# Kernel optimization log

Hardware: AMD Instinct MI355X
Metric: run time of the kernel (lower is better)

## Reference

```python
import jax, jax.numpy as jnp
import numpy as np

B, N, C, F = 8, 2048, 256, 128

def setup_inputs() -> dict:
    key = jax.random.key(0)
    ks = jax.random.split(key, 5)
    s = 0.02
    return {
        "x": jax.random.normal(ks[0], (B, N, C), dtype=jnp.float32),
        "Wf": jax.random.normal(ks[1], (C, F), dtype=jnp.float32) * s,
        "bf": jnp.zeros((F,), jnp.float32),
        "Wg": jax.random.normal(ks[2], (C, F), dtype=jnp.float32) * s,
        "bg": jnp.zeros((F,), jnp.float32),
        "Wh": jax.random.normal(ks[3], (C, F), dtype=jnp.float32) * s,
        "bh": jnp.zeros((F,), jnp.float32),
        "Wv": jax.random.normal(ks[4], (F, F), dtype=jnp.float32) * s,
        "bv": jnp.zeros((F,), jnp.float32),
    }

def reference(x, Wf, bf, Wg, bg, Wh, bh, Wv, bv):
    # 1x1 Conv1D == pointwise dense projection
    fx = x @ Wf + bf            # [B, N, F]
    gx = x @ Wg + bg            # [B, N, F]
    hx = x @ Wh + bh            # [B, N, F]
    # alpha = softmax(fx @ gx^T) over last axis -> [B, N, N]
    alpha = jax.nn.softmax(jnp.einsum('bnf,bmf->bnm', fx, gx), axis=-1)
    # o = hx^T @ alpha -> [B, F, N]
    o = jnp.einsum('bnf,bnm->bfm', hx, alpha)
    # faithful to original: RESHAPE (not transpose) to [B, N, F]
    o = o.reshape(B, N, F)
    return o @ Wv + bv          # [B, N, F]
```

## Files before the change

kernel.cpp:

```cpp
#include <hip/hip_runtime.h>
#include <hip/hip_bf16.h>


constexpr int Bb = 8, Nn = 2048, Cc = 256, Ff = 128;
constexpr long BNF = (long)Bb * Nn * Ff;
constexpr long BN  = (long)Bb * Nn;

typedef __bf16 bf16x8 __attribute__((ext_vector_type(8)));
typedef float  f32x4  __attribute__((ext_vector_type(4)));

__device__ inline unsigned short f2bf(float x) {
    unsigned u = __float_as_uint(x);
    unsigned r = (u + 0x7fffu + ((u >> 16) & 1u)) >> 16;
    return (unsigned short)r;
}
__device__ inline float bf2f(unsigned short h) {
    return __uint_as_float(((unsigned)h) << 16);
}


__global__ __launch_bounds__(256) void k_prepw(
    const float* __restrict__ W0, const float* __restrict__ W1,
    const float* __restrict__ W2,
    ushort* __restrict__ wth, ushort* __restrict__ wtl)
{
    __shared__ float ls[64][132];
    const float* W = (blockIdx.y == 0) ? W0 : (blockIdx.y == 1) ? W1 : W2;
    const int k0 = blockIdx.x * 64;
    const int t = threadIdx.x;
    const float4* src = (const float4*)(W + (size_t)k0 * 128);
    #pragma unroll
    for (int i = 0; i < 8; ++i) {
        int idx = t + 256 * i;
        int r = idx >> 5, c4 = idx & 31;
        *(float4*)&ls[r][c4 * 4] = src[idx];
    }
    __syncthreads();
    const int f = t >> 1, half = t & 1;
    __align__(16) ushort hb[32], lb[32];
    #pragma unroll
    for (int j = 0; j < 32; ++j) {
        float v = ls[half * 32 + j][f];
        ushort h = f2bf(v);
        hb[j] = h;
        lb[j] = f2bf(v - bf2f(h));
    }
    size_t base = ((size_t)blockIdx.y * 128 + f) * 256 + k0 + half * 32;
    #pragma unroll
    for (int j = 0; j < 4; ++j) {
        *(uint4*)&wth[base + j * 8] = *(const uint4*)&hb[j * 8];
        *(uint4*)&wtl[base + j * 8] = *(const uint4*)&lb[j * 8];
    }
}

__global__ __launch_bounds__(256) void k_prepwv(
    const float* __restrict__ Wv,
    ushort* __restrict__ wvth, ushort* __restrict__ wvtl)
{
    __shared__ float ls[64][132];
    const int k0 = blockIdx.x * 64;
    const int t = threadIdx.x;
    const float4* src = (const float4*)(Wv + (size_t)k0 * 128);
    #pragma unroll
    for (int i = 0; i < 8; ++i) {
        int idx = t + 256 * i;
        int r = idx >> 5, c4 = idx & 31;
        *(float4*)&ls[r][c4 * 4] = src[idx];
    }
    __syncthreads();
    const int f = t >> 1, half = t & 1;
    __align__(16) ushort hb[32], lb[32];
    #pragma unroll
    for (int j = 0; j < 32; ++j) {
        float v = ls[half * 32 + j][f];
        ushort h = f2bf(v);
        hb[j] = h;
        lb[j] = f2bf(v - bf2f(h));
    }
    size_t base = (size_t)f * 128 + k0 + half * 32;
    #pragma unroll
    for (int j = 0; j < 4; ++j) {
        *(uint4*)&wvth[base + j * 8] = *(const uint4*)&hb[j * 8];
        *(uint4*)&wvtl[base + j * 8] = *(const uint4*)&lb[j * 8];
    }
}

__global__ __launch_bounds__(512) void k_projm2(
    const float* __restrict__ x,
    const ushort* __restrict__ wth, const ushort* __restrict__ wtl,
    const float* __restrict__ b0, const float* __restrict__ b1,
    const float* __restrict__ b2,
    ushort* __restrict__ fxh, ushort* __restrict__ fxl,
    ushort* __restrict__ gxh, ushort* __restrict__ gxl,
    float* __restrict__ hxt)
{
    __shared__ ushort xsh[64][264], xsl[64][264];
    __shared__ float pmf[64][132];
    ushort (*pm)[136] = (ushort(*)[136])pmf;

    const int t = threadIdx.x;
    const long row0 = (long)blockIdx.x * 64;
    const int wid = t >> 6, lane = t & 63;
    const int wy = wid & 1, wx = wid >> 1;
    const int col = lane & 15, quad = lane >> 4;

    {
        #pragma unroll
        for (int i = 0; i < 8; ++i) {
            int idx = t + 512 * i;
            int r = idx >> 6, c4 = idx & 63;
            float4 v = *(const float4*)&x[(row0 + r) * 256 + c4 * 4];
            ushort4 h, l;
            h.x = f2bf(v.x); l.x = f2bf(v.x - bf2f(h.x));
            h.y = f2bf(v.y); l.y = f2bf(v.y - bf2f(h.y));
            h.z = f2bf(v.z); l.z = f2bf(v.z - bf2f(h.z));
            h.w = f2bf(v.w); l.w = f2bf(v.w - bf2f(h.w));
            *(ushort4*)&xsh[r][c4 * 4] = h;
            *(ushort4*)&xsl[r][c4 * 4] = l;
        }
    }
    __syncthreads();

    for (int y = 0; y < 3; ++y) {
        const ushort* Wh = wth + (size_t)y * 128 * 256;
        const ushort* Wl = wtl + (size_t)y * 128 * 256;
        const float* bias = (y == 0) ? b0 : (y == 1) ? b1 : b2;

        f32x4 acc[2][2];
        #pragma unroll
        for (int i = 0; i < 2; ++i)
            #pragma unroll
            for (int j = 0; j < 2; ++j) acc[i][j] = (f32x4){0.f, 0.f, 0.f, 0.f};

        #pragma unroll
        for (int kk = 0; kk < 8; ++kk) {
            const int ko = kk * 32 + quad * 8;
            bf16x8 ah[2], al[2], bh[2], bl[2];
            #pragma unroll
            for (int tn = 0; tn < 2; ++tn) {
                int r = wy * 32 + tn * 16 + col;
                ah[tn] = *(const bf16x8*)&xsh[r][ko];
                al[tn] = *(const bf16x8*)&xsl[r][ko];
            }
            #pragma unroll
            for (int tf = 0; tf < 2; ++tf) {
                int f = wx * 32 + tf * 16 + col;
                bh[tf] = *(const bf16x8*)&Wh[(size_t)f * 256 + ko];
                bl[tf] = *(const bf16x8*)&Wl[(size_t)f * 256 + ko];
            }
            #pragma unroll
            for (int tn = 0; tn < 2; ++tn)
                #pragma unroll
                for (int tf = 0; tf < 2; ++tf) {
                    acc[tn][tf] = __builtin_amdgcn_mfma_f32_16x16x32_bf16(ah[tn], bh[tf], acc[tn][tf], 0, 0, 0);
                    acc[tn][tf] = __builtin_amdgcn_mfma_f32_16x16x32_bf16(ah[tn], bl[tf], acc[tn][tf], 0, 0, 0);
                    acc[tn][tf] = __builtin_amdgcn_mfma_f32_16x16x32_bf16(al[tn], bh[tf], acc[tn][tf], 0, 0, 0);
                }
        }

        float v[2][2][4];
        #pragma unroll
        for (int tf = 0; tf < 2; ++tf) {
            float bb = bias[wx * 32 + tf * 16 + col];
            #pragma unroll
            for (int tn = 0; tn < 2; ++tn)
                #pragma unroll
                for (int r = 0; r < 4; ++r) v[tn][tf][r] = acc[tn][tf][r] + bb;
        }

        if (y == 2) {
            float* ob = hxt + (row0 >> 11) * (size_t)128 * 2048;
            int n0 = (int)(row0 & 2047);
            #pragma unroll
            for (int tn = 0; tn < 2; ++tn) {
                int n = n0 + wy * 32 + tn * 16 + quad * 4;
                #pragma unroll
                for (int tf = 0; tf < 2; ++tf) {
                    int f = wx * 32 + tf * 16 + col;
                    f32x4 vv = {v[tn][tf][0], v[tn][tf][1], v[tn][tf][2], v[tn][tf][3]};
                    *(f32x4*)&ob[(size_t)f * 2048 + n] = vv;
                }
            }
        } else {
            ushort* oh = (y == 0) ? fxh : gxh;
            ushort* ol = (y == 0) ? fxl : gxl;
            __syncthreads();
            #pragma unroll
            for (int tn = 0; tn < 2; ++tn)
                #pragma unroll
                for (int tf = 0; tf < 2; ++tf)
                    #pragma unroll
                    for (int r = 0; r < 4; ++r)
                        pm[wy * 32 + tn * 16 + quad * 4 + r][wx * 32 + tf * 16 + col] = f2bf(v[tn][tf][r]);
            __syncthreads();
            #pragma unroll
            for (int i = 0; i < 2; ++i) {
                int idx = t + 512 * i;
                int r = idx >> 4, c = idx & 15;
                *(uint4*)&oh[(row0 + r) * 128 + c * 8] = *(const uint4*)&pm[r][c * 8];
            }
            __syncthreads();
            #pragma unroll
            for (int tn = 0; tn < 2; ++tn)
                #pragma unroll
                for (int tf = 0; tf < 2; ++tf)
                    #pragma unroll
                    for (int r = 0; r < 4; ++r) {
                        float hv = bf2f(f2bf(v[tn][tf][r]));
                        pm[wy * 32 + tn * 16 + quad * 4 + r][wx * 32 + tf * 16 + col] = f2bf(v[tn][tf][r] - hv);
                    }
            __syncthreads();
            #pragma unroll
            for (int i = 0; i < 2; ++i) {
                int idx = t + 512 * i;
                int r = idx >> 4, c = idx & 15;
                *(uint4*)&ol[(row0 + r) * 128 + c * 8] = *(const uint4*)&pm[r][c * 8];
            }
            __syncthreads();
        }
    }
}

__global__ __launch_bounds__(512, 4) void k_score3(
    const ushort* __restrict__ fxh, const ushort* __restrict__ fxl,
    const ushort* __restrict__ gxh, const ushort* __restrict__ gxl,
    ushort* __restrict__ Pt, float* __restrict__ linv)
{
    __shared__ ushort gsh[64][136], gsl[64][136];
    __shared__ __align__(16) ushort fsbuf[2 * 64 * 136];
    __shared__ float lsum[64];
    ushort* fsh = fsbuf;
    ushort* fsl = fsbuf + 64 * 136;
    ushort* pm  = fsbuf;

    const int t = threadIdx.x;
    const int n0g = blockIdx.x * 64;
    const int b = n0g >> 11;
    const int n0 = n0g & 2047;
    const int wid = t >> 6, lane = t & 63;
    const int wy = wid & 1, wx = wid >> 1;
    const int col = lane & 15, quad = lane >> 4;

    {
        const uint4* sh = (const uint4*)(fxh + (size_t)n0g * 128);
        const uint4* sl = (const uint4*)(fxl + (size_t)n0g * 128);
        #pragma unroll
        for (int i = 0; i < 2; ++i) {
            int idx = t + 512 * i;
            int r = idx >> 4, c = idx & 15;
            *(uint4*)&fsh[r * 136 + c * 8] = sh[idx];
            *(uint4*)&fsl[r * 136 + c * 8] = sl[idx];
        }
        if (t < 64) lsum[t] = 0.f;
    }
    __syncthreads();

    bf16x8 Ah[4][2], Al[4][2];
    #pragma unroll
    for (int kk = 0; kk < 4; ++kk) {
        const int ko = kk * 32 + quad * 8;
        #pragma unroll
        for (int tn = 0; tn < 2; ++tn) {
            int r = wy * 32 + tn * 16 + col;
            Ah[kk][tn] = *(const bf16x8*)&fsh[r * 136 + ko];
            Al[kk][tn] = *(const bf16x8*)&fsl[r * 136 + ko];
        }
    }

    float rs[2][4] = {};
    const ushort* gbh = gxh + (size_t)b * 2048 * 128;
    const ushort* gbl = gxl + (size_t)b * 2048 * 128;
    ushort* Pb = Pt + (size_t)b * 2048 * 2048;

    for (int mt = 0; mt < 32; ++mt) {
        __syncthreads();
        {
            const uint4* sh = (const uint4*)(gbh + (size_t)mt * 64 * 128);
            const uint4* sl = (const uint4*)(gbl + (size_t)mt * 64 * 128);
            #pragma unroll
            for (int i = 0; i < 2; ++i) {
                int idx = t + 512 * i;
                int r = idx >> 4, c = idx & 15;
                *(uint4*)&gsh[r][c * 8] = sh[idx];
                *(uint4*)&gsl[r][c * 8] = sl[idx];
            }
        }
        __syncthreads();

        f32x4 acc[2];
        acc[0] = (f32x4){0.f, 0.f, 0.f, 0.f};
        acc[1] = (f32x4){0.f, 0.f, 0.f, 0.f};

        #pragma unroll
        for (int kk = 0; kk < 4; ++kk) {
            const int ko = kk * 32 + quad * 8;
            int r = wx * 16 + col;
            bf16x8 bh = *(const bf16x8*)&gsh[r][ko];
            bf16x8 bl = *(const bf16x8*)&gsl[r][ko];
            #pragma unroll
            for (int tn = 0; tn < 2; ++tn) {
                acc[tn] = __builtin_amdgcn_mfma_f32_16x16x32_bf16(Ah[kk][tn], bh, acc[tn], 0, 0, 0);
                acc[tn] = __builtin_amdgcn_mfma_f32_16x16x32_bf16(Ah[kk][tn], bl, acc[tn], 0, 0, 0);
                acc[tn] = __builtin_amdgcn_mfma_f32_16x16x32_bf16(Al[kk][tn], bh, acc[tn], 0, 0, 0);
            }
        }

        #pragma unroll
        for (int tn = 0; tn < 2; ++tn) {
            float e0 = __expf(acc[tn][0]);
            float e1 = __expf(acc[tn][1]);
            float e2 = __expf(acc[tn][2]);
            float e3 = __expf(acc[tn][3]);
            rs[tn][0] += e0; rs[tn][1] += e1; rs[tn][2] += e2; rs[tn][3] += e3;
            ushort4 pk;
            pk.x = f2bf(e0); pk.y = f2bf(e1); pk.z = f2bf(e2); pk.w = f2bf(e3);
            int ml = wx * 16 + col;
            int nl = wy * 32 + tn * 16 + quad * 4;
            *(ushort4*)&pm[ml * 72 + nl] = pk;
        }
        __syncthreads();
        {
            int r = t >> 3, c = t & 7;
            *(uint4*)&Pb[(size_t)(mt * 64 + r) * 2048 + n0 + c * 8] = *(const uint4*)&pm[r * 72 + c * 8];
        }
    }

    #pragma unroll
    for (int off = 1; off < 16; off <<= 1)
        #pragma unroll
        for (int tn = 0; tn < 2; ++tn)
            #pragma unroll
            for (int r = 0; r < 4; ++r) rs[tn][r] += __shfl_xor(rs[tn][r], off);
    if (col == 0) {
        #pragma unroll
        for (int tn = 0; tn < 2; ++tn)
            #pragma unroll
            for (int r = 0; r < 4; ++r)
                atomicAdd(&lsum[wy * 32 + tn * 16 + quad * 4 + r], rs[tn][r]);
    }
    __syncthreads();
    if (t < 64) linv[n0g + t] = 1.0f / lsum[t];
}

__global__ __launch_bounds__(256) void k_scaleh2(
    const float* __restrict__ hxt, const float* __restrict__ linv,
    ushort* __restrict__ hth, ushort* __restrict__ htl)
{
    const int t = threadIdx.x;
    const int bf = blockIdx.x;
    const int b = bf >> 7;
    const size_t base = (size_t)bf * 2048;
    const float* L = linv + (size_t)b * 2048;
    const int n = t * 8;
    float4 v0 = *(const float4*)&hxt[base + n];
    float4 v1 = *(const float4*)&hxt[base + n + 4];
    float4 l0 = *(const float4*)&L[n];
    float4 l1 = *(const float4*)&L[n + 4];
    float w[8] = {v0.x * l0.x, v0.y * l0.y, v0.z * l0.z, v0.w * l0.w,
                  v1.x * l1.x, v1.y * l1.y, v1.z * l1.z, v1.w * l1.w};
    __align__(16) ushort hb[8], lb[8];
    #pragma unroll
    for (int j = 0; j < 8; ++j) {
        ushort h = f2bf(w[j]);
        hb[j] = h;
        lb[j] = f2bf(w[j] - bf2f(h));
    }
    *(uint4*)&hth[base + n] = *(const uint4*)&hb[0];
    *(uint4*)&htl[base + n] = *(const uint4*)&lb[0];
}

__global__ __launch_bounds__(256) void k_pv3(
    const ushort* __restrict__ Pt,
    const ushort* __restrict__ hth, const ushort* __restrict__ htl,
    float* __restrict__ op0, float* __restrict__ op1)
{
    __shared__ ushort ps[32][72];
    __shared__ ushort hsh[128][72], hsl[128][72];
    const int t = threadIdx.x;
    const int ks = blockIdx.x & 1;
    const int m0g = (blockIdx.x >> 1) * 32;
    const int b = m0g >> 11, m0 = m0g & 2047;
    const int wx = t >> 6;
    const int lane = t & 63;
    const int col = lane & 15, quad = lane >> 4;
    const int nbase = ks * 1024;

    const ushort* Pb = Pt + ((size_t)b * 2048 + m0) * 2048 + nbase;
    const ushort* Hh = hth + (size_t)b * 128 * 2048 + nbase;
    const ushort* Hl = htl + (size_t)b * 128 * 2048 + nbase;

    f32x4 acc[2][2];
    #pragma unroll
    for (int i = 0; i < 2; ++i)
        #pragma unroll
        for (int j = 0; j < 2; ++j) acc[i][j] = (f32x4){0.f, 0.f, 0.f, 0.f};

    for (int nt = 0; nt < 16; ++nt) {
        __syncthreads();
        {
            int r = t >> 3, c = t & 7;
            *(uint4*)&ps[r][c * 8] = *(const uint4*)&Pb[(size_t)r * 2048 + nt * 64 + c * 8];
            #pragma unroll
            for (int i = 0; i < 4; ++i) {
                int idx = t + 256 * i;
                int rr = idx >> 3, cc = idx & 7;
                size_t g = (size_t)rr * 2048 + nt * 64 + cc * 8;
                *(uint4*)&hsh[rr][cc * 8] = *(const uint4*)&Hh[g];
                *(uint4*)&hsl[rr][cc * 8] = *(const uint4*)&Hl[g];
            }
        }
        __syncthreads();

        #pragma unroll
        for (int kk = 0; kk < 2; ++kk) {
            const int ko = kk * 32 + quad * 8;
            bf16x8 a[2], bh[2], bl[2];
            #pragma unroll
            for (int tm = 0; tm < 2; ++tm)
                a[tm] = *(const bf16x8*)&ps[tm * 16 + col][ko];
            #pragma unroll
            for (int tf = 0; tf < 2; ++tf) {
                int r = wx * 32 + tf * 16 + col;
                bh[tf] = *(const bf16x8*)&hsh[r][ko];
                bl[tf] = *(const bf16x8*)&hsl[r][ko];
            }
            #pragma unroll
            for (int tm = 0; tm < 2; ++tm)
                #pragma unroll
                for (int tf = 0; tf < 2; ++tf) {
                    acc[tm][tf] = __builtin_amdgcn_mfma_f32_16x16x32_bf16(a[tm], bh[tf], acc[tm][tf], 0, 0, 0);
                    acc[tm][tf] = __builtin_amdgcn_mfma_f32_16x16x32_bf16(a[tm], bl[tf], acc[tm][tf], 0, 0, 0);
                }
        }
    }

    float* op = (ks == 0) ? op0 : op1;
    float* ob = op + (size_t)b * 128 * 2048;
    #pragma unroll
    for (int tm = 0; tm < 2; ++tm) {
        int m = m0 + tm * 16 + quad * 4;
        #pragma unroll
        for (int tf = 0; tf < 2; ++tf) {
            int f = wx * 32 + tf * 16 + col;
            *(f32x4*)&ob[(size_t)f * 2048 + m] = acc[tm][tf];
        }
    }
}

__global__ __launch_bounds__(512) void k_final_m2(
    const float* __restrict__ op0, const float* __restrict__ op1,
    const ushort* __restrict__ wvth, const ushort* __restrict__ wvtl,
    const float* __restrict__ bv, float* __restrict__ out)
{
    __shared__ ushort ash[64][136], asl[64][136];
    __shared__ float pmf[64][132];
    const int t = threadIdx.x;
    const long row0 = (long)blockIdx.x * 64;
    const int wid = t >> 6, lane = t & 63;
    const int wy = wid & 1, wx = wid >> 1;
    const int col = lane & 15, quad = lane >> 4;

    {
        const float4* s0 = (const float4*)(op0 + row0 * 128);
        const float4* s1 = (const float4*)(op1 + row0 * 128);
        #pragma unroll
        for (int i = 0; i < 4; ++i) {
            int idx = t + 512 * i;
            float4 a = s0[idx], bq = s1[idx];
            float v0 = a.x + bq.x, v1 = a.y + bq.y, v2 = a.z + bq.z, v3 = a.w + bq.w;
            ushort4 h, l;
            h.x = f2bf(v0); l.x = f2bf(v0 - bf2f(h.x));
            h.y = f2bf(v1); l.y = f2bf(v1 - bf2f(h.y));
            h.z = f2bf(v2); l.z = f2bf(v2 - bf2f(h.z));
            h.w = f2bf(v3); l.w = f2bf(v3 - bf2f(h.w));
            int r = idx >> 5, c4 = idx & 31;
            *(ushort4*)&ash[r][c4 * 4] = h;
            *(ushort4*)&asl[r][c4 * 4] = l;
        }
    }
    __syncthreads();

    f32x4 acc[2][2];
    #pragma unroll
    for (int i = 0; i < 2; ++i)
        #pragma unroll
        for (int j = 0; j < 2; ++j) acc[i][j] = (f32x4){0.f, 0.f, 0.f, 0.f};

    #pragma unroll
    for (int kk = 0; kk < 4; ++kk) {
        const int ko = kk * 32 + quad * 8;
        bf16x8 ah[2], al[2], bh[2], bl[2];
        #pragma unroll
        for (int tn = 0; tn < 2; ++tn) {
            int r = wy * 32 + tn * 16 + col;
            ah[tn] = *(const bf16x8*)&ash[r][ko];
            al[tn] = *(const bf16x8*)&asl[r][ko];
        }
        #pragma unroll
        for (int tf = 0; tf < 2; ++tf) {
            int f = wx * 32 + tf * 16 + col;
            bh[tf] = *(const bf16x8*)&wvth[(size_t)f * 128 + ko];
            bl[tf] = *(const bf16x8*)&wvtl[(size_t)f * 128 + ko];
        }
        #pragma unroll
        for (int tn = 0; tn < 2; ++tn)
            #pragma unroll
            for (int tf = 0; tf < 2; ++tf) {
                acc[tn][tf] = __builtin_amdgcn_mfma_f32_16x16x32_bf16(ah[tn], bh[tf], acc[tn][tf], 0, 0, 0);
                acc[tn][tf] = __builtin_amdgcn_mfma_f32_16x16x32_bf16(ah[tn], bl[tf], acc[tn][tf], 0, 0, 0);
                acc[tn][tf] = __builtin_amdgcn_mfma_f32_16x16x32_bf16(al[tn], bh[tf], acc[tn][tf], 0, 0, 0);
            }
    }

    #pragma unroll
    for (int tf = 0; tf < 2; ++tf) {
        int f = wx * 32 + tf * 16 + col;
        float bb = bv[f];
        #pragma unroll
        for (int tn = 0; tn < 2; ++tn)
            #pragma unroll
            for (int r = 0; r < 4; ++r)
                pmf[wy * 32 + tn * 16 + quad * 4 + r][f] = acc[tn][tf][r] + bb;
    }
    __syncthreads();
    #pragma unroll
    for (int i = 0; i < 4; ++i) {
        int idx = t + 512 * i;
        int r = idx >> 5, c4 = idx & 31;
        *(float4*)&out[(row0 + r) * 128 + c4 * 4] = *(const float4*)&pmf[r][c4 * 4];
    }
}


__global__ __launch_bounds__(256) void k_proj(
    const float* __restrict__ x,
    const float* __restrict__ W0, const float* __restrict__ b0,
    const float* __restrict__ W1, const float* __restrict__ b1,
    const float* __restrict__ W2, const float* __restrict__ b2,
    float* __restrict__ o0, float* __restrict__ o1, float* __restrict__ o2)
{
    const float* W; const float* bias; float* out;
    if (blockIdx.y == 0)      { W = W0; bias = b0; out = o0; }
    else if (blockIdx.y == 1) { W = W1; bias = b1; out = o1; }
    else                      { W = W2; bias = b2; out = o2; }

    __shared__ float xs[32][Cc];
    const int t = threadIdx.x;
    const long row0 = (long)blockIdx.x * 32;
    const float4* xg = (const float4*)(x + row0 * Cc);
    float4* xs4 = (float4*)xs;
    #pragma unroll
    for (int i = 0; i < 8; ++i) xs4[t + 256 * i] = xg[t + 256 * i];
    __syncthreads();

    const int cg = t & 31;
    const int rq = t >> 5;
    float acc[4][4] = {};
    const float4* W4 = (const float4*)W;
    for (int k4 = 0; k4 < Cc / 4; ++k4) {
        float4 av[4];
        #pragma unroll
        for (int i = 0; i < 4; ++i) av[i] = *(const float4*)&xs[4 * rq + i][k4 * 4];
        float4 wv4[4];
        #pragma unroll
        for (int kk = 0; kk < 4; ++kk) wv4[kk] = W4[(size_t)(4 * k4 + kk) * (Ff / 4) + cg];
        #pragma unroll
        for (int kk = 0; kk < 4; ++kk) {
            float4 w = wv4[kk];
            #pragma unroll
            for (int i = 0; i < 4; ++i) {
                float a = (kk == 0) ? av[i].x : (kk == 1) ? av[i].y : (kk == 2) ? av[i].z : av[i].w;
                acc[i][0] += a * w.x; acc[i][1] += a * w.y;
                acc[i][2] += a * w.z; acc[i][3] += a * w.w;
            }
        }
    }
    float4 bb = ((const float4*)bias)[cg];
    #pragma unroll
    for (int i = 0; i < 4; ++i) {
        float4 r;
        r.x = acc[i][0] + bb.x; r.y = acc[i][1] + bb.y;
        r.z = acc[i][2] + bb.z; r.w = acc[i][3] + bb.w;
        ((float4*)(out + (row0 + 4 * rq + i) * Ff))[cg] = r;
    }
}

__global__ __launch_bounds__(256) void k_stats(
    const float* __restrict__ fx, const float* __restrict__ gx,
    float* __restrict__ linv)
{
    __shared__ float fs[64][132];
    __shared__ float gs[128][132];
    const int t = threadIdx.x;
    const int n0 = blockIdx.x * 64;
    const int b = n0 / Nn;
    const float* gxb = gx + (long)b * Nn * Ff;
    {
        const float4* src = (const float4*)(fx + (long)n0 * Ff);
        #pragma unroll
        for (int i = 0; i < 8; ++i) {
            int idx = t + 256 * i;
            int r = idx >> 5, c4 = idx & 31;
            *(float4*)&fs[r][c4 * 4] = src[idx];
        }
    }
    const int ty = t >> 4;
    const int tx = t & 15;
    float lsum[4] = {0.f, 0.f, 0.f, 0.f};
    for (int mt = 0; mt < Nn / 128; ++mt) {
        __syncthreads();
        {
            const float4* src = (const float4*)(gxb + (long)mt * 128 * Ff);
            #pragma unroll
            for (int i = 0; i < 16; ++i) {
                int idx = t + 256 * i;
                int r = idx >> 5, c4 = idx & 31;
                *(float4*)&gs[r][c4 * 4] = src[idx];
            }
        }
        __syncthreads();
        float s[4][8] = {};
        for (int k4 = 0; k4 < 32; ++k4) {
            float4 a[4], g4[8];
            #pragma unroll
            for (int i = 0; i < 4; ++i) a[i] = *(const float4*)&fs[ty + 16 * i][k4 * 4];
            #pragma unroll
            for (int j = 0; j < 8; ++j) g4[j] = *(const float4*)&gs[tx + 16 * j][k4 * 4];
            #pragma unroll
            for (int i = 0; i < 4; ++i)
                #pragma unroll
                for (int j = 0; j < 8; ++j)
                    s[i][j] += a[i].x * g4[j].x + a[i].y * g4[j].y
                             + a[i].z * g4[j].z + a[i].w * g4[j].w;
        }
        #pragma unroll
        for (int i = 0; i < 4; ++i) {
            float e = 0.f;
            #pragma unroll
            for (int j = 0; j < 8; ++j) e += __expf(s[i][j]);
            lsum[i] += e;
        }
    }
    #pragma unroll
    for (int off = 1; off < 16; off <<= 1)
        #pragma unroll
        for (int i = 0; i < 4; ++i) lsum[i] += __shfl_xor(lsum[i], off);
    if (tx == 0)
        #pragma unroll
        for (int i = 0; i < 4; ++i) linv[n0 + ty + 16 * i] = 1.0f / lsum[i];
}

__global__ __launch_bounds__(256) void k_attnpv(
    const float* __restrict__ fx, const float* __restrict__ gx,
    const float* __restrict__ hx, const float* __restrict__ linv,
    float* __restrict__ o)
{
    __shared__ float gs[64][132];
    __shared__ float fs[64][132];
    __shared__ float hs[64][132];
    __shared__ float ps[64][68];
    __shared__ float li[64];
    const int t = threadIdx.x;
    const int m0g = blockIdx.x * 64;
    const int b = m0g / Nn;
    const int m0 = m0g - b * Nn;
    const float* fxb = fx + (long)b * Nn * Ff;
    const float* hxb = hx + (long)b * Nn * Ff;
    {
        const float4* src = (const float4*)(gx + (long)m0g * Ff);
        #pragma unroll
        for (int i = 0; i < 8; ++i) {
            int idx = t + 256 * i;
            int r = idx >> 5, c4 = idx & 31;
            *(float4*)&gs[r][c4 * 4] = src[idx];
        }
    }
    const int ty = t >> 4;
    const int tx = t & 15;
    float acc[4][8] = {};
    for (int nt = 0; nt < Nn / 64; ++nt) {
        __syncthreads();
        {
            const float4* srcf = (const float4*)(fxb + (long)nt * 64 * Ff);
            const float4* srch = (const float4*)(hxb + (long)nt * 64 * Ff);
            #pragma unroll
            for (int i = 0; i < 8; ++i) {
                int idx = t + 256 * i;
                int r = idx >> 5, c4 = idx & 31;
                *(float4*)&fs[r][c4 * 4] = srcf[idx];
                *(float4*)&hs[r][c4 * 4] = srch[idx];
            }
            if (t < 64) li[t] = linv[(long)b * Nn + nt * 64 + t];
        }
        __syncthreads();
        float s[4][4] = {};
        for (int k4 = 0; k4 < 32; ++k4) {
            float4 a[4], g4[4];
            #pragma unroll
            for (int i = 0; i < 4; ++i) a[i] = *(const float4*)&fs[ty + 16 * i][k4 * 4];
            #pragma unroll
            for (int j = 0; j < 4; ++j) g4[j] = *(const float4*)&gs[tx + 16 * j][k4 * 4];
            #pragma unroll
            for (int i = 0; i < 4; ++i)
                #pragma unroll
                for (int j = 0; j < 4; ++j)
                    s[i][j] += a[i].x * g4[j].x + a[i].y * g4[j].y
                             + a[i].z * g4[j].z + a[i].w * g4[j].w;
        }
        #pragma unroll
        for (int i = 0; i < 4; ++i) {
            float lv = li[ty + 16 * i];
            #pragma unroll
            for (int j = 0; j < 4; ++j)
                ps[ty + 16 * i][tx + 16 * j] = __expf(s[i][j]) * lv;
        }
        __syncthreads();
        #pragma unroll 4
        for (int n = 0; n < 64; ++n) {
            float4 h0 = *(const float4*)&hs[n][tx * 8];
            float4 h1 = *(const float4*)&hs[n][tx * 8 + 4];
            float pv[4];
            #pragma unroll
            for (int im = 0; im < 4; ++im) pv[im] = ps[n][ty + 16 * im];
            #pragma unroll
            for (int im = 0; im < 4; ++im) {
                acc[im][0] += pv[im] * h0.x; acc[im][1] += pv[im] * h0.y;
                acc[im][2] += pv[im] * h0.z; acc[im][3] += pv[im] * h0.w;
                acc[im][4] += pv[im] * h1.x; acc[im][5] += pv[im] * h1.y;
                acc[im][6] += pv[im] * h1.z; acc[im][7] += pv[im] * h1.w;
            }
        }
    }
    float* ob = o + (size_t)b * Ff * Nn;
    #pragma unroll
    for (int im = 0; im < 4; ++im) {
        int m = m0 + ty + 16 * im;
        #pragma unroll
        for (int jf = 0; jf < 8; ++jf)
            ob[(size_t)(tx * 8 + jf) * Nn + m] = acc[im][jf];
    }
}

__global__ __launch_bounds__(256) void k_final(
    const float* __restrict__ in2, const float* __restrict__ Wv,
    const float* __restrict__ bv, float* __restrict__ out)
{
    __shared__ float xs[32][132];
    const int t = threadIdx.x;
    const long row0 = (long)blockIdx.x * 32;
    {
        const float4* src = (const float4*)(in2 + row0 * Ff);
        #pragma unroll
        for (int i = 0; i < 4; ++i) {
            int idx = t + 256 * i;
            int r = idx >> 5, c4 = idx & 31;
            *(float4*)&xs[r][c4 * 4] = src[idx];
        }
    }
    __syncthreads();

    const int cg = t & 31;
    const int rq = t >> 5;
    float acc[4][4] = {};
    const float4* W4 = (const float4*)Wv;
    for (int k4 = 0; k4 < 32; ++k4) {
        float4 av[4];
        #pragma unroll
        for (int i = 0; i < 4; ++i) av[i] = *(const float4*)&xs[4 * rq + i][k4 * 4];
        float4 wv4[4];
        #pragma unroll
        for (int kk = 0; kk < 4; ++kk) wv4[kk] = W4[(size_t)(4 * k4 + kk) * 32 + cg];
        #pragma unroll
        for (int kk = 0; kk < 4; ++kk) {
            float4 w = wv4[kk];
            #pragma unroll
            for (int i = 0; i < 4; ++i) {
                float a = (kk == 0) ? av[i].x : (kk == 1) ? av[i].y : (kk == 2) ? av[i].z : av[i].w;
                acc[i][0] += a * w.x; acc[i][1] += a * w.y;
                acc[i][2] += a * w.z; acc[i][3] += a * w.w;
            }
        }
    }
    float4 bb = ((const float4*)bv)[cg];
    #pragma unroll
    for (int i = 0; i < 4; ++i) {
        float4 r;
        r.x = acc[i][0] + bb.x; r.y = acc[i][1] + bb.y;
        r.z = acc[i][2] + bb.z; r.w = acc[i][3] + bb.w;
        ((float4*)(out + (row0 + 4 * rq + i) * Ff))[cg] = r;
    }
}


extern "C" void kernel_launch(void* const* d_in, const int* in_sizes, int n_in,
                              void* d_out, int out_size, void* d_ws, size_t ws_size,
                              hipStream_t stream) {
    const float* x  = (const float*)d_in[0];
    const float* Wf = (const float*)d_in[1];
    const float* bf = (const float*)d_in[2];
    const float* Wg = (const float*)d_in[3];
    const float* bg = (const float*)d_in[4];
    const float* Wh = (const float*)d_in[5];
    const float* bh = (const float*)d_in[6];
    const float* Wv = (const float*)d_in[7];
    const float* bv = (const float*)d_in[8];
    float* out = (float*)d_out;

    const size_t sz_hxt  = (size_t)BNF * 4;
    const size_t sz_linv = (size_t)BN * 4;
    const size_t sz_bf   = (size_t)BNF * 2;
    const size_t sz_Pt   = (size_t)Bb * Nn * Nn * 2;
    const size_t sz_wt   = (size_t)3 * 128 * 256 * 2;
    const size_t sz_wv   = (size_t)128 * 128 * 2;
    const size_t need = sz_hxt + sz_linv + 8 * sz_bf + sz_Pt + 2 * sz_wt + 2 * sz_wv;

    if (ws_size >= need) {
        char* p = (char*)d_ws;
        float* hxt   = (float*)p;            p += sz_hxt;
        float* linv  = (float*)p;            p += sz_linv;
        ushort* fxh  = (ushort*)p;           p += sz_bf;
        ushort* fxl  = (ushort*)p;           p += sz_bf;
        ushort* gxh  = (ushort*)p;           p += sz_bf;
        ushort* gxl  = (ushort*)p;           p += sz_bf;
        ushort* hth  = (ushort*)p;           p += sz_bf;
        ushort* htl  = (ushort*)p;           p += sz_bf;
        float* op0   = hxt;
        float* op1   = (float*)fxh;
        p += 2 * sz_bf;
        ushort* wth  = (ushort*)p;           p += sz_wt;
        ushort* wtl  = (ushort*)p;           p += sz_wt;
        ushort* wvth = (ushort*)p;           p += sz_wv;
        ushort* wvtl = (ushort*)p;           p += sz_wv;
        ushort* Pt   = (ushort*)p;

        k_prepw   <<<dim3(4, 3), 256, 0, stream>>>(Wf, Wg, Wh, wth, wtl);
        k_prepwv  <<<2, 256, 0, stream>>>(Wv, wvth, wvtl);
        k_projm2  <<<BN / 64, 512, 0, stream>>>(x, wth, wtl, bf, bg, bh,
                                                fxh, fxl, gxh, gxl, hxt);
        k_score3  <<<BN / 64, 512, 0, stream>>>(fxh, fxl, gxh, gxl, Pt, linv);
        k_scaleh2 <<<Bb * Ff, 256, 0, stream>>>(hxt, linv, hth, htl);
        k_pv3     <<<(BN / 32) * 2, 256, 0, stream>>>(Pt, hth, htl, op0, op1);
        k_final_m2<<<BN / 64, 512, 0, stream>>>(op0, op1, wvth, wvtl, bv, out);
    } else {
        float* ws   = (float*)d_ws;
        float* fx   = ws;
        float* gx   = fx + BNF;
        float* hx   = gx + BNF;
        float* linv = hx + BNF;
        float* o    = linv + BN;
        k_proj  <<<dim3(BN / 32, 3), 256, 0, stream>>>(x, Wf, bf, Wg, bg, Wh, bh, fx, gx, hx);
        k_stats <<<BN / 64, 256, 0, stream>>>(fx, gx, linv);
        k_attnpv<<<BN / 64, 256, 0, stream>>>(fx, gx, hx, linv, o);
        k_final <<<BN / 32, 256, 0, stream>>>(o, Wv, bv, out);
    }
}
```

Measured before the change: 208.5 us.

## Split score kernel over key blocks and load MFMA operands directly from global

The score kernel now splits the key dimension across four blocks per query tile, writing partial row sums that the scale kernel adds up before taking the reciprocal. Both the score and PV kernels drop their LDS staging of operands and load MFMA fragments straight from global memory, which removes most __syncthreads barriers and shrinks LDS use. The score output buffer is double-buffered in LDS. In exchange, global/L2 traffic per wave goes up and loads are less coalesced, and the partial sums need extra workspace.

```diff
diff --git a/kernel.cpp b/kernel.cpp
--- a/kernel.cpp
+++ b/kernel.cpp
@@ -221,39 +221,23 @@
     }
 }
 
-__global__ __launch_bounds__(512, 4) void k_score3(
+__global__ __launch_bounds__(512, 4) void k_score4(
     const ushort* __restrict__ fxh, const ushort* __restrict__ fxl,
     const ushort* __restrict__ gxh, const ushort* __restrict__ gxl,
-    ushort* __restrict__ Pt, float* __restrict__ linv)
-{
-    __shared__ ushort gsh[64][136], gsl[64][136];
-    __shared__ __align__(16) ushort fsbuf[2 * 64 * 136];
+    ushort* __restrict__ Pt, float* __restrict__ lsum4)
+{
+    __shared__ ushort pm[2][64][72];
     __shared__ float lsum[64];
-    ushort* fsh = fsbuf;
-    ushort* fsl = fsbuf + 64 * 136;
-    ushort* pm  = fsbuf;
-
     const int t = threadIdx.x;
     const int n0g = blockIdx.x * 64;
+    const int ms = blockIdx.y;
     const int b = n0g >> 11;
     const int n0 = n0g & 2047;
     const int wid = t >> 6, lane = t & 63;
     const int wy = wid & 1, wx = wid >> 1;
     const int col = lane & 15, quad = lane >> 4;
 
-    {
-        const uint4* sh = (const uint4*)(fxh + (size_t)n0g * 128);
-        const uint4* sl = (const uint4*)(fxl + (size_t)n0g * 128);
-        #pragma unroll
-        for (int i = 0; i < 2; ++i) {
-            int idx = t + 512 * i;
-            int r = idx >> 4, c = idx & 15;
-            *(uint4*)&fsh[r * 136 + c * 8] = sh[idx];
-            *(uint4*)&fsl[r * 136 + c * 8] = sl[idx];
-        }
-        if (t < 64) lsum[t] = 0.f;
-    }
-    __syncthreads();
+    if (t < 64) lsum[t] = 0.f;
 
     bf16x8 Ah[4][2], Al[4][2];
     #pragma unroll
@@ -261,32 +245,20 @@
         const int ko = kk * 32 + quad * 8;
         #pragma unroll
         for (int tn = 0; tn < 2; ++tn) {
-            int r = wy * 32 + tn * 16 + col;
-            Ah[kk][tn] = *(const bf16x8*)&fsh[r * 136 + ko];
-            Al[kk][tn] = *(const bf16x8*)&fsl[r * 136 + ko];
-        }
-    }
+            size_t off = (size_t)(n0g + wy * 32 + tn * 16 + col) * 128 + ko;
+            Ah[kk][tn] = *(const bf16x8*)&fxh[off];
+            Al[kk][tn] = *(const bf16x8*)&fxl[off];
+        }
+    }
+    __syncthreads();
 
     float rs[2][4] = {};
     const ushort* gbh = gxh + (size_t)b * 2048 * 128;
     const ushort* gbl = gxl + (size_t)b * 2048 * 128;
     ushort* Pb = Pt + (size_t)b * 2048 * 2048;
 
-    for (int mt = 0; mt < 32; ++mt) {
-        __syncthreads();
-        {
-            const uint4* sh = (const uint4*)(gbh + (size_t)mt * 64 * 128);
-            const uint4* sl = (const uint4*)(gbl + (size_t)mt * 64 * 128);
-            #pragma unroll
-            for (int i = 0; i < 2; ++i) {
-                int idx = t + 512 * i;
-                int r = idx >> 4, c = idx & 15;
-                *(uint4*)&gsh[r][c * 8] = sh[idx];
-                *(uint4*)&gsl[r][c * 8] = sl[idx];
-            }
-        }
-        __syncthreads();
-
+    for (int mt = 0; mt < 8; ++mt) {
+        const int m0 = ms * 512 + mt * 64;
         f32x4 acc[2];
         acc[0] = (f32x4){0.f, 0.f, 0.f, 0.f};
         acc[1] = (f32x4){0.f, 0.f, 0.f, 0.f};
@@ -294,9 +266,9 @@
         #pragma unroll
         for (int kk = 0; kk < 4; ++kk) {
             const int ko = kk * 32 + quad * 8;
-            int r = wx * 16 + col;
-            bf16x8 bh = *(const bf16x8*)&gsh[r][ko];
-            bf16x8 bl = *(const bf16x8*)&gsl[r][ko];
+            size_t off = (size_t)(m0 + wx * 16 + col) * 128 + ko;
+            bf16x8 bh = *(const bf16x8*)&gbh[off];
+            bf16x8 bl = *(const bf16x8*)&gbl[off];
             #pragma unroll
             for (int tn = 0; tn < 2; ++tn) {
                 acc[tn] = __builtin_amdgcn_mfma_f32_16x16x32_bf16(Ah[kk][tn], bh, acc[tn], 0, 0, 0);
@@ -305,6 +277,7 @@
             }
         }
 
+        ushort (*pmc)[72] = pm[mt & 1];
         #pragma unroll
         for (int tn = 0; tn < 2; ++tn) {
             float e0 = __expf(acc[tn][0]);
@@ -314,14 +287,12 @@
             rs[tn][0] += e0; rs[tn][1] += e1; rs[tn][2] += e2; rs[tn][3] += e3;
             ushort4 pk;
             pk.x = f2bf(e0); pk.y = f2bf(e1); pk.z = f2bf(e2); pk.w = f2bf(e3);
-            int ml = wx * 16 + col;
-            int nl = wy * 32 + tn * 16 + quad * 4;
-            *(ushort4*)&pm[ml * 72 + nl] = pk;
+            *(ushort4*)&pmc[wx * 16 + col][wy * 32 + tn * 16 + quad * 4] = pk;
         }
         __syncthreads();
         {
             int r = t >> 3, c = t & 7;
-            *(uint4*)&Pb[(size_t)(mt * 64 + r) * 2048 + n0 + c * 8] = *(const uint4*)&pm[r * 72 + c * 8];
+            *(uint4*)&Pb[(size_t)(m0 + r) * 2048 + n0 + c * 8] = *(const uint4*)&pmc[r][c * 8];
         }
     }
 
@@ -339,46 +310,51 @@
                 atomicAdd(&lsum[wy * 32 + tn * 16 + quad * 4 + r], rs[tn][r]);
     }
     __syncthreads();
-    if (t < 64) linv[n0g + t] = 1.0f / lsum[t];
-}
-
-__global__ __launch_bounds__(256) void k_scaleh2(
-    const float* __restrict__ hxt, const float* __restrict__ linv,
+    if (t < 64) lsum4[(size_t)ms * BN + n0g + t] = lsum[t];
+}
+
+__global__ __launch_bounds__(256) void k_scaleh3(
+    const float* __restrict__ hxt, const float* __restrict__ lsum4,
     ushort* __restrict__ hth, ushort* __restrict__ htl)
 {
     const int t = threadIdx.x;
     const int bf = blockIdx.x;
     const int b = bf >> 7;
     const size_t base = (size_t)bf * 2048;
-    const float* L = linv + (size_t)b * 2048;
+    const size_t gn = (size_t)b * 2048 + t * 8;
     const int n = t * 8;
+
     float4 v0 = *(const float4*)&hxt[base + n];
     float4 v1 = *(const float4*)&hxt[base + n + 4];
-    float4 l0 = *(const float4*)&L[n];
-    float4 l1 = *(const float4*)&L[n + 4];
-    float w[8] = {v0.x * l0.x, v0.y * l0.y, v0.z * l0.z, v0.w * l0.w,
-                  v1.x * l1.x, v1.y * l1.y, v1.z * l1.z, v1.w * l1.w};
+    float l[8] = {};
+    #pragma unroll
+    for (int ms = 0; ms < 4; ++ms) {
+        float4 a = *(const float4*)&lsum4[(size_t)ms * BN + gn];
+        float4 c = *(const float4*)&lsum4[(size_t)ms * BN + gn + 4];
+        l[0] += a.x; l[1] += a.y; l[2] += a.z; l[3] += a.w;
+        l[4] += c.x; l[5] += c.y; l[6] += c.z; l[7] += c.w;
+    }
+    float vv[8] = {v0.x, v0.y, v0.z, v0.w, v1.x, v1.y, v1.z, v1.w};
     __align__(16) ushort hb[8], lb[8];
     #pragma unroll
     for (int j = 0; j < 8; ++j) {
-        ushort h = f2bf(w[j]);
+        float w = vv[j] * (1.0f / l[j]);
+        ushort h = f2bf(w);
         hb[j] = h;
-        lb[j] = f2bf(w[j] - bf2f(h));
+        lb[j] = f2bf(w - bf2f(h));
     }
     *(uint4*)&hth[base + n] = *(const uint4*)&hb[0];
     *(uint4*)&htl[base + n] = *(const uint4*)&lb[0];
 }
 
-__global__ __launch_bounds__(256) void k_pv3(
+__global__ __launch_bounds__(256) void k_pv4(
     const ushort* __restrict__ Pt,
     const ushort* __restrict__ hth, const ushort* __restrict__ htl,
     float* __restrict__ op0, float* __restrict__ op1)
 {
-    __shared__ ushort ps[32][72];
-    __shared__ ushort hsh[128][72], hsl[128][72];
-    const int t = threadIdx.x;
-    const int ks = blockIdx.x & 1;
-    const int m0g = (blockIdx.x >> 1) * 32;
+    const int t = threadIdx.x;
+    const int ks = blockIdx.y;
+    const int m0g = blockIdx.x * 32;
     const int b = m0g >> 11, m0 = m0g & 2047;
     const int wx = t >> 6;
     const int lane = t & 63;
@@ -396,33 +372,18 @@
         for (int j = 0; j < 2; ++j) acc[i][j] = (f32x4){0.f, 0.f, 0.f, 0.f};
 
     for (int nt = 0; nt < 16; ++nt) {
-        __syncthreads();
-        {
-            int r = t >> 3, c = t & 7;
-            *(uint4*)&ps[r][c * 8] = *(const uint4*)&Pb[(size_t)r * 2048 + nt * 64 + c * 8];
-            #pragma unroll
-            for (int i = 0; i < 4; ++i) {
-                int idx = t + 256 * i;
-                int rr = idx >> 3, cc = idx & 7;
-                size_t g = (size_t)rr * 2048 + nt * 64 + cc * 8;
-                *(uint4*)&hsh[rr][cc * 8] = *(const uint4*)&Hh[g];
-                *(uint4*)&hsl[rr][cc * 8] = *(const uint4*)&Hl[g];
-            }
-        }
-        __syncthreads();
-
         #pragma unroll
         for (int kk = 0; kk < 2; ++kk) {
-            const int ko = kk * 32 + quad * 8;
+            const int ko = nt * 64 + kk * 32 + quad * 8;
             bf16x8 a[2], bh[2], bl[2];
             #pragma unroll
             for (int tm = 0; tm < 2; ++tm)
-                a[tm] = *(const bf16x8*)&ps[tm * 16 + col][ko];
+                a[tm] = *(const bf16x8*)&Pb[(size_t)(tm * 16 + col) * 2048 + ko];
             #pragma unroll
             for (int tf = 0; tf < 2; ++tf) {
-                int r = wx * 32 + tf * 16 + col;
-                bh[tf] = *(const bf16x8*)&hsh[r][ko];
-                bl[tf] = *(const bf16x8*)&hsl[r][ko];
+                size_t ho = (size_t)(wx * 32 + tf * 16 + col) * 2048 + ko;
+                bh[tf] = *(const bf16x8*)&Hh[ho];
+                bl[tf] = *(const bf16x8*)&Hl[ho];
             }
             #pragma unroll
             for (int tm = 0; tm < 2; ++tm)
@@ -817,13 +778,14 @@
     if (ws_size >= need) {
         char* p = (char*)d_ws;
         float* hxt   = (float*)p;            p += sz_hxt;
-        float* linv  = (float*)p;            p += sz_linv;
+        p += sz_linv;
         ushort* fxh  = (ushort*)p;           p += sz_bf;
         ushort* fxl  = (ushort*)p;           p += sz_bf;
         ushort* gxh  = (ushort*)p;           p += sz_bf;
         ushort* gxl  = (ushort*)p;           p += sz_bf;
         ushort* hth  = (ushort*)p;           p += sz_bf;
         ushort* htl  = (ushort*)p;           p += sz_bf;
+        float* lsum4 = (float*)p;
         float* op0   = hxt;
         float* op1   = (float*)fxh;
         p += 2 * sz_bf;
@@ -837,9 +799,9 @@
         k_prepwv  <<<2, 256, 0, stream>>>(Wv, wvth, wvtl);
         k_projm2  <<<BN / 64, 512, 0, stream>>>(x, wth, wtl, bf, bg, bh,
                                                 fxh, fxl, gxh, gxl, hxt);
-        k_score3  <<<BN / 64, 512, 0, stream>>>(fxh, fxl, gxh, gxl, Pt, linv);
-        k_scaleh2 <<<Bb * Ff, 256, 0, stream>>>(hxt, linv, hth, htl);
-        k_pv3     <<<(BN / 32) * 2, 256, 0, stream>>>(Pt, hth, htl, op0, op1);
+        k_score4  <<<dim3(BN / 64, 4), 512, 0, stream>>>(fxh, fxl, gxh, gxl, Pt, lsum4);
+        k_scaleh3 <<<Bb * Ff, 256, 0, stream>>>(hxt, lsum4, hth, htl);
+        k_pv4     <<<dim3(BN / 32, 2), 256, 0, stream>>>(Pt, hth, htl, op0, op1);
         k_final_m2<<<BN / 64, 512, 0, stream>>>(op0, op1, wvth, wvtl, bv, out);
     } else {
         float* ws   = (float*)d_ws;
```

New measurement: 290.1 us. 1.39x slower.
